# Kernel tuning notes

Hardware: AMD Instinct MI355X
Metric: run time of the kernel (lower is better)

The kernel has to match this reference:

```python
import jax, jax.numpy as jnp
import numpy as np

C = 256
R = 16
CR = C // R  # 16

def setup_inputs() -> dict:
    key = jax.random.key(0)
    k1, k2, k3 = jax.random.split(key, 3)
    x = jax.random.normal(k1, (16, C, 128, 128), dtype=jnp.float32)
    # 1x1 conv weights expressed as channel matmuls
    w1 = jax.random.normal(k2, (CR, C), dtype=jnp.float32) * (1.0 / np.sqrt(C))
    b1 = jnp.zeros((CR,), dtype=jnp.float32)
    w2 = jax.random.normal(k3, (C, CR), dtype=jnp.float32) * (1.0 / np.sqrt(CR))
    b2 = jnp.zeros((C,), dtype=jnp.float32)
    return {"x": x, "w1": w1, "b1": b1, "w2": w2, "b2": b2}

def reference(x, w1, b1, w2, b2):
    # global average pool over H,W -> [B, C]
    y = jnp.mean(x, axis=(2, 3))
    # 1x1 conv MLP: [B,C] @ [C,CR]^T -> relu -> [B,CR] @ [CR,C]^T -> sigmoid
    y = jax.nn.relu(jnp.einsum('bc,rc->br', y, w1) + b1)
    y = jax.nn.sigmoid(jnp.einsum('br,cr->bc', y, w2) + b2)
    # channel gating broadcast back onto x
    return x * y[:, :, None, None]
```

## Files before the change

### kernel.cpp

```cpp
#include <hip/hip_runtime.h>
#include <math.h>

#define PLANE 16384
#define NPLANES 4096
#define NB 16
#define NC 256
#define NR 16

typedef float vfloat4 __attribute__((ext_vector_type(4)));

__global__ __launch_bounds__(256, 8) void pool_kernel(const float* __restrict__ x,
                                                      float* __restrict__ mean) {
    const size_t base = (size_t)blockIdx.x * PLANE;
    const vfloat4* xp = (const vfloat4*)(x + base);
    const int tid = threadIdx.x;
    float s = 0.f;
    #pragma unroll
    for (int h = 0; h < 2; ++h) {
        vfloat4 v[8];
        #pragma unroll
        for (int j = 0; j < 8; ++j) v[j] = xp[tid + (h * 8 + j) * 256];
        #pragma unroll
        for (int j = 0; j < 8; ++j) s += (v[j].x + v[j].y) + (v[j].z + v[j].w);
    }
    #pragma unroll
    for (int o = 32; o > 0; o >>= 1) s += __shfl_down(s, o, 64);
    __shared__ float wsum[4];
    if ((tid & 63) == 0) wsum[tid >> 6] = s;
    __syncthreads();
    if (tid == 0) {
        mean[blockIdx.x] = ((wsum[0] + wsum[1]) + (wsum[2] + wsum[3])) * (1.0f / (float)PLANE);
    }
}

__global__ __launch_bounds__(256) void gate_kernel(const float* __restrict__ mean,
                                                   const float* __restrict__ w1,
                                                   const float* __restrict__ b1,
                                                   const float* __restrict__ w2,
                                                   const float* __restrict__ b2,
                                                   float* __restrict__ gate) {
    const int b = blockIdx.x;
    const int tid = threadIdx.x;
    const int wave = tid >> 6;
    const int lane = tid & 63;

    __shared__ float hsh[NR];
    {
        const vfloat4 yv = ((const vfloat4*)(mean + b * NC))[lane];
        #pragma unroll
        for (int k = 0; k < 4; ++k) {
            const int r = wave * 4 + k;
            const vfloat4 wv = ((const vfloat4*)(w1 + r * NC))[lane];
            float p = yv.x * wv.x + yv.y * wv.y + yv.z * wv.z + yv.w * wv.w;
            #pragma unroll
            for (int o = 32; o > 0; o >>= 1) p += __shfl_down(p, o, 64);
            if (lane == 0) hsh[r] = fmaxf(p + b1[r], 0.f);
        }
    }
    __syncthreads();
    const int c = tid;
    float a = b2[c];
    #pragma unroll
    for (int r = 0; r < NR; ++r) a += hsh[r] * w2[c * NR + r];
    gate[b * NC + c] = 1.0f / (1.0f + expf(-a));
}

__global__ __launch_bounds__(256, 8) void scale_kernel(const float* __restrict__ x,
                                                       const float* __restrict__ gate,
                                                       float* __restrict__ out) {
    const int i = blockIdx.x;
    const int plane = (4088 - (i & ~7)) + (i & 7);
    const float g = gate[plane];
    const size_t base = (size_t)plane * PLANE;
    const vfloat4* xp = (const vfloat4*)(x + base);
    vfloat4* op = (vfloat4*)(out + base);
    const int tid = threadIdx.x;
    #pragma unroll
    for (int h = 0; h < 2; ++h) {
        vfloat4 v[8];
        #pragma unroll
        for (int j = 0; j < 8; ++j) v[j] = xp[tid + (h * 8 + j) * 256];
        #pragma unroll
        for (int j = 0; j < 8; ++j) {
            vfloat4 w = v[j];
            w.x *= g; w.y *= g; w.z *= g; w.w *= g;
            __builtin_nontemporal_store(w, op + tid + (h * 8 + j) * 256);
        }
    }
}

extern "C" void kernel_launch(void* const* d_in, const int* in_sizes, int n_in,
                              void* d_out, int out_size, void* d_ws, size_t ws_size,
                              hipStream_t stream) {
    const float* x  = (const float*)d_in[0];
    const float* w1 = (const float*)d_in[1];
    const float* b1 = (const float*)d_in[2];
    const float* w2 = (const float*)d_in[3];
    const float* b2 = (const float*)d_in[4];
    float* out = (float*)d_out;

    float* mean = (float*)d_ws;
    float* gate = mean + NPLANES;

    pool_kernel<<<NPLANES, 256, 0, stream>>>(x, mean);
    gate_kernel<<<NB, 256, 0, stream>>>(mean, w1, b1, w2, b2, gate);
    scale_kernel<<<NPLANES, 256, 0, stream>>>(x, gate, out);
}
```

Measured before the change: 483.2 us.

## Fuse pool, gate MLP and scale into one kernel with inter-block flags

Replaces the three launches with one kernel of 2048 blocks, each handling two planes. Each block pools its planes and publishes the means. One block per batch waits for all 256 means, computes the gate MLP and raises a flag. Every block then waits on that flag and re-reads its planes to scale them. The aim is to remove launch gaps and re-read x while it is more likely to still be in cache. This relies on all blocks being resident at once, which the 8-blocks-per-CU launch bound is meant to guarantee; otherwise the spin-waits could deadlock.

```diff
diff --git a/kernel.cpp b/kernel.cpp
--- a/kernel.cpp
+++ b/kernel.cpp
@@ -6,85 +6,113 @@
 #define NB 16
 #define NC 256
 #define NR 16
+#define GRID 2048
 
 typedef float vfloat4 __attribute__((ext_vector_type(4)));
 
-__global__ __launch_bounds__(256, 8) void pool_kernel(const float* __restrict__ x,
-                                                      float* __restrict__ mean) {
-    const size_t base = (size_t)blockIdx.x * PLANE;
-    const vfloat4* xp = (const vfloat4*)(x + base);
+__global__ __launch_bounds__(256, 8) void fused_kernel(
+    const float* __restrict__ x,
+    const float* __restrict__ w1, const float* __restrict__ b1,
+    const float* __restrict__ w2, const float* __restrict__ b2,
+    float* __restrict__ out,
+    float* __restrict__ mean, float* __restrict__ gate,
+    unsigned int* __restrict__ ready, unsigned int* __restrict__ gflag)
+{
+    const int i   = blockIdx.x;
     const int tid = threadIdx.x;
-    float s = 0.f;
+    const int wave = tid >> 6, lane = tid & 63;
+    const int p0 = i * 2;
+    const int b  = p0 >> 8;
+
+    __shared__ float wsum[4];
+    __shared__ float hsh[NR];
+    __shared__ float msh[NC];
+
     #pragma unroll
-    for (int h = 0; h < 2; ++h) {
-        vfloat4 v[8];
+    for (int q = 0; q < 2; ++q) {
+        const int p = p0 + q;
+        const vfloat4* xp = (const vfloat4*)(x + (size_t)p * PLANE);
+        float s = 0.f;
         #pragma unroll
-        for (int j = 0; j < 8; ++j) v[j] = xp[tid + (h * 8 + j) * 256];
+        for (int h = 0; h < 2; ++h) {
+            vfloat4 v[8];
+            #pragma unroll
+            for (int j = 0; j < 8; ++j) v[j] = xp[tid + (h * 8 + j) * 256];
+            #pragma unroll
+            for (int j = 0; j < 8; ++j) s += (v[j].x + v[j].y) + (v[j].z + v[j].w);
+        }
         #pragma unroll
-        for (int j = 0; j < 8; ++j) s += (v[j].x + v[j].y) + (v[j].z + v[j].w);
+        for (int o = 32; o > 0; o >>= 1) s += __shfl_down(s, o, 64);
+        if (lane == 0) wsum[wave] = s;
+        __syncthreads();
+        if (tid == 0) {
+            float m = ((wsum[0] + wsum[1]) + (wsum[2] + wsum[3])) * (1.0f / (float)PLANE);
+            __hip_atomic_store(&mean[p], m, __ATOMIC_RELAXED, __HIP_MEMORY_SCOPE_AGENT);
+        }
+        __syncthreads();
     }
-    #pragma unroll
-    for (int o = 32; o > 0; o >>= 1) s += __shfl_down(s, o, 64);
-    __shared__ float wsum[4];
-    if ((tid & 63) == 0) wsum[tid >> 6] = s;
-    __syncthreads();
-    if (tid == 0) {
-        mean[blockIdx.x] = ((wsum[0] + wsum[1]) + (wsum[2] + wsum[3])) * (1.0f / (float)PLANE);
-    }
-}
+    if (tid == 0)
+        __hip_atomic_fetch_add(&ready[b], 2u, __ATOMIC_RELEASE, __HIP_MEMORY_SCOPE_AGENT);
 
-__global__ __launch_bounds__(256) void gate_kernel(const float* __restrict__ mean,
-                                                   const float* __restrict__ w1,
-                                                   const float* __restrict__ b1,
-                                                   const float* __restrict__ w2,
-                                                   const float* __restrict__ b2,
-                                                   float* __restrict__ gate) {
-    const int b = blockIdx.x;
-    const int tid = threadIdx.x;
-    const int wave = tid >> 6;
-    const int lane = tid & 63;
-
-    __shared__ float hsh[NR];
-    {
-        const vfloat4 yv = ((const vfloat4*)(mean + b * NC))[lane];
+    if ((i & 127) == 127) {
+        if (tid == 0) {
+            while (__hip_atomic_load(&ready[b], __ATOMIC_ACQUIRE, __HIP_MEMORY_SCOPE_AGENT)
+                   < (unsigned)NC)
+                __builtin_amdgcn_s_sleep(4);
+        }
+        __syncthreads();
+        msh[tid] = __hip_atomic_load(&mean[b * NC + tid], __ATOMIC_RELAXED,
+                                     __HIP_MEMORY_SCOPE_AGENT);
+        __syncthreads();
         #pragma unroll
         for (int k = 0; k < 4; ++k) {
             const int r = wave * 4 + k;
             const vfloat4 wv = ((const vfloat4*)(w1 + r * NC))[lane];
-            float p = yv.x * wv.x + yv.y * wv.y + yv.z * wv.z + yv.w * wv.w;
+            float p = msh[4 * lane + 0] * wv.x + msh[4 * lane + 1] * wv.y
+                    + msh[4 * lane + 2] * wv.z + msh[4 * lane + 3] * wv.w;
             #pragma unroll
             for (int o = 32; o > 0; o >>= 1) p += __shfl_down(p, o, 64);
             if (lane == 0) hsh[r] = fmaxf(p + b1[r], 0.f);
         }
+        __syncthreads();
+        {
+            const int c = tid;
+            float a = b2[c];
+            #pragma unroll
+            for (int r = 0; r < NR; ++r) a += hsh[r] * w2[c * NR + r];
+            float g = 1.0f / (1.0f + expf(-a));
+            __hip_atomic_store(&gate[b * NC + c], g, __ATOMIC_RELAXED,
+                               __HIP_MEMORY_SCOPE_AGENT);
+        }
+        __syncthreads();
+        if (tid == 0)
+            __hip_atomic_store(&gflag[b], 1u, __ATOMIC_RELEASE, __HIP_MEMORY_SCOPE_AGENT);
+    }
+
+    if (tid == 0) {
+        while (__hip_atomic_load(&gflag[b], __ATOMIC_ACQUIRE, __HIP_MEMORY_SCOPE_AGENT) == 0u)
+            __builtin_amdgcn_s_sleep(4);
     }
     __syncthreads();
-    const int c = tid;
-    float a = b2[c];
     #pragma unroll
-    for (int r = 0; r < NR; ++r) a += hsh[r] * w2[c * NR + r];
-    gate[b * NC + c] = 1.0f / (1.0f + expf(-a));
-}
-
-__global__ __launch_bounds__(256, 8) void scale_kernel(const float* __restrict__ x,
-                                                       const float* __restrict__ gate,
-                                                       float* __restrict__ out) {
-    const int i = blockIdx.x;
-    const int plane = (4088 - (i & ~7)) + (i & 7);
-    const float g = gate[plane];
-    const size_t base = (size_t)plane * PLANE;
-    const vfloat4* xp = (const vfloat4*)(x + base);
-    vfloat4* op = (vfloat4*)(out + base);
-    const int tid = threadIdx.x;
-    #pragma unroll
-    for (int h = 0; h < 2; ++h) {
-        vfloat4 v[8];
+    for (int q = 0; q < 2; ++q) {
+        const int p = p0 + q;
+        const float g = __hip_atomic_load(&gate[p], __ATOMIC_RELAXED,
+                                          __HIP_MEMORY_SCOPE_AGENT);
+        const size_t base = (size_t)p * PLANE;
+        const vfloat4* xp = (const vfloat4*)(x + base);
+        vfloat4* op = (vfloat4*)(out + base);
         #pragma unroll
-        for (int j = 0; j < 8; ++j) v[j] = xp[tid + (h * 8 + j) * 256];
-        #pragma unroll
-        for (int j = 0; j < 8; ++j) {
-            vfloat4 w = v[j];
-            w.x *= g; w.y *= g; w.z *= g; w.w *= g;
-            __builtin_nontemporal_store(w, op + tid + (h * 8 + j) * 256);
+        for (int h = 0; h < 2; ++h) {
+            vfloat4 v[8];
+            #pragma unroll
+            for (int j = 0; j < 8; ++j) v[j] = xp[tid + (h * 8 + j) * 256];
+            #pragma unroll
+            for (int j = 0; j < 8; ++j) {
+                vfloat4 w = v[j];
+                w.x *= g; w.y *= g; w.z *= g; w.w *= g;
+                __builtin_nontemporal_store(w, op + tid + (h * 8 + j) * 256);
+            }
         }
     }
 }
@@ -101,8 +129,11 @@
 
     float* mean = (float*)d_ws;
     float* gate = mean + NPLANES;
+    unsigned int* ready = (unsigned int*)(gate + NPLANES);
+    unsigned int* gflag = ready + NB;
 
-    pool_kernel<<<NPLANES, 256, 0, stream>>>(x, mean);
-    gate_kernel<<<NB, 256, 0, stream>>>(mean, w1, b1, w2, b2, gate);
-    scale_kernel<<<NPLANES, 256, 0, stream>>>(x, gate, out);
+    hipMemsetAsync(ready, 0, 2 * NB * sizeof(unsigned int), stream);
+
+    fused_kernel<<<GRID, 256, 0, stream>>>(x, w1, b1, w2, b2, out,
+                                           mean, gate, ready, gflag);
 }
```

Result: slower. 788.0 us (+63.1%).
